# Performance work log

Measured on AMD Instinct MI355X. Metric: run time of the kernel, lower is better.

The kernel has to match this reference:

```python
import jax, jax.numpy as jnp
import numpy as np

B, T, C, H = 2, 2048, 1024, 16
HD = C // H  # head dim = 64


def setup_inputs() -> dict:
    key = jax.random.key(0)
    k1, k2, k3, k4, k5 = jax.random.split(key, 5)
    s = 0.02
    return {
        "x": jax.random.normal(k1, (B, T, C), dtype=jnp.float32),
        "W_attn": jax.random.normal(k2, (3 * C, C), dtype=jnp.float32) * s,
        "b_attn": jax.random.normal(k3, (3 * C,), dtype=jnp.float32) * s,
        "W_proj": jax.random.normal(k4, (C, C), dtype=jnp.float32) * s,
        "b_proj": jax.random.normal(k5, (C,), dtype=jnp.float32) * s,
    }


def reference(x, W_attn, b_attn, W_proj, b_proj):
    Bs, Ts, Cs = x.shape
    # QKV projection (torch Linear: x @ W.T + b)
    qkv = x @ W_attn.T + b_attn  # (B, T, 3C)
    q, k, v = jnp.split(qkv, 3, axis=2)
    # (B, H, T, HD)
    q = q.reshape(Bs, Ts, H, HD).transpose(0, 2, 1, 3)
    k = k.reshape(Bs, Ts, H, HD).transpose(0, 2, 1, 3)
    v = v.reshape(Bs, Ts, H, HD).transpose(0, 2, 1, 3)
    scale = 1.0 / np.sqrt(HD).astype(np.float32)
    att = jnp.einsum("bhqd,bhkd->bhqk", q, k) * scale
    causal = jnp.tril(jnp.ones((Ts, Ts), dtype=bool))
    att = jnp.where(causal[None, None], att, -jnp.inf)
    att = jax.nn.softmax(att, axis=-1)
    y = jnp.einsum("bhqk,bhkd->bhqd", att, v)
    y = y.transpose(0, 2, 1, 3).reshape(Bs, Ts, Cs)
    return y @ W_proj.T + b_proj
```

## Files before the change

### kernel.cpp

```cpp
#include <hip/hip_runtime.h>


#define B_   2
#define T_   2048
#define C_   1024
#define H_   16
#define HD_  64
#define BT_  (B_ * T_)
#define C3_  (3 * C_)
#define NT_  (T_ / 64)
#define SCL_ 0.18033688f

typedef __attribute__((ext_vector_type(8))) __bf16 bf16x8;
typedef __attribute__((ext_vector_type(4))) float  f32x4;
typedef __attribute__((ext_vector_type(8))) unsigned short u16x8;

__device__ __forceinline__ unsigned short f2bf(float f) {
    unsigned int u = __float_as_uint(f);
    u = (u + 0x7fffu + ((u >> 16) & 1u)) >> 16;
    return (unsigned short)u;
}
__device__ __forceinline__ unsigned short bfc(float f) {
    return __builtin_bit_cast(unsigned short, (__bf16)f);
}

__device__ __forceinline__ size_t vphys(size_t idx) {
    return (idx >> 10) * 3072 + 2048 + (idx & 1023);
}

#define NX8  (BT_ * C_ / 8)
#define NWA8 (C3_ * C_ / 8)
#define NWP8 (C_ * C_ / 8)
#define NB8  (C3_ / 8)
#define NTOT (NX8 + NWA8 + NWP8 + NB8)
__global__ __launch_bounds__(256) void cvt3(const float* __restrict__ x,
                                            const float* __restrict__ wa,
                                            const float* __restrict__ wp,
                                            const float* __restrict__ ba,
                                            unsigned short* __restrict__ ox,
                                            unsigned short* __restrict__ owa,
                                            unsigned short* __restrict__ owp,
                                            float* __restrict__ obs) {
    int i = blockIdx.x * 256 + threadIdx.x;
    if (i >= NTOT) return;
    if (i >= NX8 + NWA8 + NWP8) {
        int jb = i - (NX8 + NWA8 + NWP8);
        int e  = jb * 8;
        float s = (e < C_) ? SCL_ : 1.0f;
        const float4* p = (const float4*)(ba + e);
        float4 f0 = p[0], f1 = p[1];
        float4* o = (float4*)(obs + e);
        o[0] = make_float4(f0.x * s, f0.y * s, f0.z * s, f0.w * s);
        o[1] = make_float4(f1.x * s, f1.y * s, f1.z * s, f1.w * s);
        return;
    }
    const float* in;
    unsigned short* out;
    int j;
    float s = 1.0f;
    if (i < NX8)             { in = x;  out = ox;  j = i; }
    else if (i < NX8 + NWA8) { in = wa; out = owa; j = i - NX8;
                               if (j < NWP8) s = SCL_; }
    else                     { in = wp; out = owp; j = i - NX8 - NWA8; }
    const float4* p = (const float4*)in;
    float4 f0 = p[j * 2];
    float4 f1 = p[j * 2 + 1];
    u16x8 o;
    o[0] = f2bf(f0.x * s); o[1] = f2bf(f0.y * s); o[2] = f2bf(f0.z * s); o[3] = f2bf(f0.w * s);
    o[4] = f2bf(f1.x * s); o[5] = f2bf(f1.y * s); o[6] = f2bf(f1.z * s); o[7] = f2bf(f1.w * s);
    ((u16x8*)out)[j] = o;
}

template<int OUT_BF16, int VSPLIT>
__global__ __launch_bounds__(256) void gemm_bt(const unsigned short* __restrict__ A,
                                               const unsigned short* __restrict__ Bm,
                                               const float* __restrict__ bias,
                                               void* __restrict__ Cv,
                                               int M, int N, int K, int nbx) {
    __shared__ __align__(16) unsigned short As[128][72];
    __shared__ __align__(16) unsigned short Bs[128][72];

    const int t    = threadIdx.x;
    const int lane = t & 63;
    const int w    = t >> 6;
    const int wr   = w & 1;
    const int wc   = w >> 1;
    const int l15  = lane & 15;
    const int lhi  = lane >> 4;

    const int nwg = gridDim.x;
    const int q8  = nwg >> 3;
    const int lin = (int)(blockIdx.x & 7) * q8 + (int)(blockIdx.x >> 3);
    const int bx  = lin % nbx;
    const int by  = lin / nbx;
    const int m0  = by * 128;
    const int n0  = bx * 128;

    f32x4 acc[4][4] = {};

    const int nk = K >> 6;
    for (int kb = 0; kb < nk; ++kb) {
        __syncthreads();
        #pragma unroll
        for (int i = 0; i < 4; ++i) {
            int g   = i * 256 + t;
            int row = g >> 3;
            int kc  = g & 7;
            uint4 va = *(const uint4*)(A  + (size_t)(m0 + row) * K + kb * 64 + kc * 8);
            *(uint4*)(&As[row][kc * 8]) = va;
            uint4 vb = *(const uint4*)(Bm + (size_t)(n0 + row) * K + kb * 64 + kc * 8);
            *(uint4*)(&Bs[row][kc * 8]) = vb;
        }
        __syncthreads();
        #pragma unroll
        for (int kk = 0; kk < 2; ++kk) {
            bf16x8 af[4], bfm[4];
            #pragma unroll
            for (int m = 0; m < 4; ++m)
                af[m] = *(const bf16x8*)(&As[wr * 64 + m * 16 + l15][kk * 32 + lhi * 8]);
            #pragma unroll
            for (int n = 0; n < 4; ++n)
                bfm[n] = *(const bf16x8*)(&Bs[wc * 64 + n * 16 + l15][kk * 32 + lhi * 8]);
            #pragma unroll
            for (int m = 0; m < 4; ++m)
                #pragma unroll
                for (int n = 0; n < 4; ++n)
                    acc[m][n] = __builtin_amdgcn_mfma_f32_16x16x32_bf16(af[m], bfm[n], acc[m][n], 0, 0, 0);
        }
    }

    if (VSPLIT && n0 >= 2048) {
        #pragma unroll
        for (int n = 0; n < 4; ++n) {
            int cg = n0 + wc * 64 + n * 16 + l15;
            float bv = bias[cg];
            int d_ = cg - 2048;
            int hh = d_ >> 6;
            int dd = d_ & 63;
            #pragma unroll
            for (int m = 0; m < 4; ++m) {
                int rg0 = m0 + wr * 64 + m * 16 + lhi * 4;
                int bb  = rg0 >> 11;
                int tt  = rg0 & 2047;
                size_t idx = ((size_t)((bb * 16 + hh) * 64 + dd)) * 2048 + tt;
                unsigned short* dst = (unsigned short*)Cv + vphys(idx);
                uint2 pk;
                pk.x = (unsigned int)f2bf(acc[m][n][0] + bv) |
                       ((unsigned int)f2bf(acc[m][n][1] + bv) << 16);
                pk.y = (unsigned int)f2bf(acc[m][n][2] + bv) |
                       ((unsigned int)f2bf(acc[m][n][3] + bv) << 16);
                *(uint2*)dst = pk;
            }
        }
    } else {
        #pragma unroll
        for (int n = 0; n < 4; ++n) {
            int cg = n0 + wc * 64 + n * 16 + l15;
            float bv = bias[cg];
            #pragma unroll
            for (int m = 0; m < 4; ++m) {
                #pragma unroll
                for (int i = 0; i < 4; ++i) {
                    int rg  = m0 + wr * 64 + m * 16 + lhi * 4 + i;
                    float v = acc[m][n][i] + bv;
                    if (OUT_BF16)
                        ((unsigned short*)Cv)[(size_t)rg * N + cg] = f2bf(v);
                    else
                        ((float*)Cv)[(size_t)rg * N + cg] = v;
                }
            }
        }
    }
}

__global__ __launch_bounds__(256) void attn_fwd(const unsigned short* __restrict__ qkv,
                                                unsigned short* __restrict__ y) {
    __shared__ __align__(16) unsigned short Ks[128][72];
    __shared__ __align__(16) unsigned short Vt[64][136];

    const int t    = threadIdx.x;
    const int lane = t & 63;
    const int wv   = t >> 6;
    const int l15  = lane & 15;
    const int lhi  = lane >> 4;
    const int b    = blockIdx.y >> 4;
    const int h    = blockIdx.y & 15;
    const size_t rowbase = (size_t)b * T_ * C3_;
    const int hoff = h * HD_;
    unsigned short* PsW = &Ks[0][0] + wv * (16 * 136);

    const unsigned short* krow = qkv + rowbase + C_ + hoff;
    const size_t vIdx0 = ((size_t)(b * 16 + h) * 64) * 2048;

    #pragma unroll 1
    for (int half = 0; half < 2; ++half) {
        const int qt = half ? (NT_ - 1 - (int)blockIdx.x) : (int)blockIdx.x;
        const int q0 = qt * 64;

        bf16x8 qf[2];
        {
            int qrow = q0 + wv * 16 + l15;
            const unsigned short* qp = qkv + rowbase + (size_t)qrow * C3_ + hoff + lhi * 8;
            qf[0] = *(const bf16x8*)(qp);
            qf[1] = *(const bf16x8*)(qp + 32);
        }

        float Mx = -1e30f, Lx = 0.f;
        f32x4 oacc[4];
        #pragma unroll
        for (int n = 0; n < 4; ++n) oacc[n] = f32x4{0.f, 0.f, 0.f, 0.f};

        const int niter = (qt + 2) >> 1;
        for (int it = 0; it < niter; ++it) {
            const int k0 = it * 128;
            __syncthreads();
            #pragma unroll
            for (int i = 0; i < 4; ++i) {
                int g   = i * 256 + t;
                int row = g >> 3;
                int kc  = g & 7;
                *(uint4*)(&Ks[row][kc * 8]) =
                    *(const uint4*)(krow + (size_t)(k0 + row) * C3_ + kc * 8);
            }
            #pragma unroll
            for (int i = 0; i < 4; ++i) {
                int g  = i * 256 + t;
                int dd = g >> 4;
                int kc = g & 15;
                size_t idx = vIdx0 + (size_t)dd * 2048 + k0 + kc * 8;
                *(u16x8*)(&Vt[dd][kc * 8]) = *(const u16x8*)(qkv + vphys(idx));
            }
            __syncthreads();

            f32x4 sacc[8];
            #pragma unroll
            for (int n = 0; n < 8; ++n) sacc[n] = f32x4{0.f, 0.f, 0.f, 0.f};
            __builtin_amdgcn_s_setprio(1);
            #pragma unroll
            for (int kk = 0; kk < 2; ++kk) {
                #pragma unroll
                for (int n = 0; n < 8; ++n) {
                    bf16x8 kf = *(const bf16x8*)(&Ks[n * 16 + l15][kk * 32 + lhi * 8]);
                    sacc[n] = __builtin_amdgcn_mfma_f32_16x16x32_bf16(kf, qf[kk], sacc[n], 0, 0, 0);
                }
            }
            __builtin_amdgcn_s_setprio(0);
            __syncthreads();

            const int qg = q0 + wv * 16 + l15;
            if (k0 + 127 > q0) {
                #pragma unroll
                for (int n = 0; n < 8; ++n) {
                    int kg = k0 + n * 16 + lhi * 4;
                    #pragma unroll
                    for (int r = 0; r < 4; ++r)
                        sacc[n][r] = (kg + r <= qg) ? sacc[n][r] : -1e30f;
                }
            }

            float vmx = sacc[0][0];
            #pragma unroll
            for (int n = 0; n < 8; ++n)
                #pragma unroll
                for (int r = 0; r < 4; ++r) vmx = fmaxf(vmx, sacc[n][r]);
            vmx = fmaxf(vmx, __shfl_xor(vmx, 16));
            vmx = fmaxf(vmx, __shfl_xor(vmx, 32));
            float Mn = fmaxf(Mx, vmx);
            float al = exp2f(Mx - Mn);
            Mx = Mn;
            float rs = 0.f;
            #pragma unroll
            for (int n = 0; n < 8; ++n)
                #pragma unroll
                for (int r = 0; r < 4; ++r) {
                    float e = exp2f(sacc[n][r] - Mn);
                    sacc[n][r] = e;
                    rs += e;
                }
            rs += __shfl_xor(rs, 16);
            rs += __shfl_xor(rs, 32);
            Lx = Lx * al + rs;

            #pragma unroll
            for (int r = 0; r < 4; ++r) {
                float ar = __shfl(al, lhi * 4 + r);
                #pragma unroll
                for (int nd = 0; nd < 4; ++nd) oacc[nd][r] *= ar;
            }

            #pragma unroll
            for (int n = 0; n < 8; ++n) {
                unsigned int lo = (unsigned int)bfc(sacc[n][0]) | ((unsigned int)bfc(sacc[n][1]) << 16);
                unsigned int hi = (unsigned int)bfc(sacc[n][2]) | ((unsigned int)bfc(sacc[n][3]) << 16);
                uint2 pk; pk.x = lo; pk.y = hi;
                *(uint2*)(PsW + l15 * 136 + n * 16 + lhi * 4) = pk;
            }
            asm volatile("s_waitcnt lgkmcnt(0)" ::: "memory");

            __builtin_amdgcn_s_setprio(1);
            #pragma unroll
            for (int kk = 0; kk < 4; ++kk) {
                bf16x8 pf = *(const bf16x8*)(PsW + l15 * 136 + kk * 32 + lhi * 8);
                #pragma unroll
                for (int nd = 0; nd < 4; ++nd) {
                    bf16x8 vf = *(const bf16x8*)(&Vt[nd * 16 + l15][kk * 32 + lhi * 8]);
                    oacc[nd] = __builtin_amdgcn_mfma_f32_16x16x32_bf16(pf, vf, oacc[nd], 0, 0, 0);
                }
            }
            __builtin_amdgcn_s_setprio(0);
        }

        #pragma unroll
        for (int i = 0; i < 4; ++i) {
            float Lr = __shfl(Lx, lhi * 4 + i);
            float rL = 1.0f / Lr;
            #pragma unroll
            for (int nd = 0; nd < 4; ++nd) {
                int qg = q0 + wv * 16 + lhi * 4 + i;
                y[(size_t)(b * T_ + qg) * C_ + hoff + nd * 16 + l15] = bfc(oacc[nd][i] * rL);
            }
        }
    }
}

extern "C" void kernel_launch(void* const* d_in, const int* in_sizes, int n_in,
                              void* d_out, int out_size, void* d_ws, size_t ws_size,
                              hipStream_t stream) {
    const float* x      = (const float*)d_in[0];
    const float* W_attn = (const float*)d_in[1];
    const float* b_attn = (const float*)d_in[2];
    const float* W_proj = (const float*)d_in[3];
    const float* b_proj = (const float*)d_in[4];
    float* out = (float*)d_out;

    char* ws = (char*)d_ws;
    unsigned short* xb   = (unsigned short*)(ws);
    unsigned short* wab  = (unsigned short*)(ws + 8388608);
    unsigned short* wpb  = (unsigned short*)(ws + 8388608 + 6291456);
    unsigned short* qkvb = (unsigned short*)(ws + 16777216);
    unsigned short* yb   = (unsigned short*)(ws + 16777216 + 25165824);
    float*          bs   = (float*)(ws + 16777216 + 25165824 + 8388608);

    cvt3<<<(NTOT + 255) / 256, 256, 0, stream>>>(x, W_attn, W_proj, b_attn, xb, wab, wpb, bs);

    gemm_bt<1, 1><<<(C3_ / 128) * (BT_ / 128), 256, 0, stream>>>(xb, wab, bs, qkvb, BT_, C3_, C_, C3_ / 128);

    attn_fwd<<<dim3(NT_ / 2, B_ * H_), 256, 0, stream>>>(qkvb, yb);

    gemm_bt<0, 0><<<(C_ / 128) * (BT_ / 128), 256, 0, stream>>>(yb, wpb, b_proj, out, BT_, C_, C_, C_ / 128);
}
```

Before: 211.0 us.

## Swizzle attention LDS tiles into fragment order and remap blocks across XCDs

Replaces the padded row-major K and transposed-V shared-memory tiles with an XOR-swizzled layout. Each MFMA fragment read becomes a contiguous 16-byte load at a precomputed offset, and the P scratch uses the same scheme. The aim is to cut LDS bank conflicts and address arithmetic in the inner loop. The grid also becomes 1D with a block-index permutation, so neighbouring head/query-pair blocks are spread across the XCDs, and a sched_barrier is added before the PV MFMAs. The risk is more complex store addressing and swizzle bugs.

```diff
diff --git a/kernel.cpp b/kernel.cpp
--- a/kernel.cpp
+++ b/kernel.cpp
@@ -175,34 +175,45 @@
 
 __global__ __launch_bounds__(256) void attn_fwd(const unsigned short* __restrict__ qkv,
                                                 unsigned short* __restrict__ y) {
-    __shared__ __align__(16) unsigned short Ks[128][72];
-    __shared__ __align__(16) unsigned short Vt[64][136];
+    __shared__ __align__(16) unsigned short KL[8192];
+    __shared__ __align__(16) unsigned short VL[8192];
 
     const int t    = threadIdx.x;
     const int lane = t & 63;
     const int wv   = t >> 6;
     const int l15  = lane & 15;
     const int lhi  = lane >> 4;
-    const int b    = blockIdx.y >> 4;
-    const int h    = blockIdx.y & 15;
+
+    const int bid = blockIdx.x;
+    const int idx = (bid >> 3) + (bid & 7) * 64;
+    const int bh  = idx >> 4;
+    const int qp  = idx & 15;
+    const int b   = bh >> 4;
+    const int h   = bh & 15;
     const size_t rowbase = (size_t)b * T_ * C3_;
     const int hoff = h * HD_;
-    unsigned short* PsW = &Ks[0][0] + wv * (16 * 136);
+
+    unsigned short* Pw = KL + wv * 2048;
+
+    int voff[4];
+    #pragma unroll
+    for (int kk = 0; kk < 4; ++kk)
+        voff[kk] = ((kk * 4 + lhi) * 16 + (l15 ^ lhi ^ ((kk & 1) << 2))) * 8;
 
     const unsigned short* krow = qkv + rowbase + C_ + hoff;
     const size_t vIdx0 = ((size_t)(b * 16 + h) * 64) * 2048;
 
     #pragma unroll 1
     for (int half = 0; half < 2; ++half) {
-        const int qt = half ? (NT_ - 1 - (int)blockIdx.x) : (int)blockIdx.x;
+        const int qt = half ? (NT_ - 1 - qp) : qp;
         const int q0 = qt * 64;
 
         bf16x8 qf[2];
         {
             int qrow = q0 + wv * 16 + l15;
-            const unsigned short* qp = qkv + rowbase + (size_t)qrow * C3_ + hoff + lhi * 8;
-            qf[0] = *(const bf16x8*)(qp);
-            qf[1] = *(const bf16x8*)(qp + 32);
+            const unsigned short* qp_ = qkv + rowbase + (size_t)qrow * C3_ + hoff + lhi * 8;
+            qf[0] = *(const bf16x8*)(qp_);
+            qf[1] = *(const bf16x8*)(qp_ + 32);
         }
 
         float Mx = -1e30f, Lx = 0.f;
@@ -217,18 +228,20 @@
             #pragma unroll
             for (int i = 0; i < 4; ++i) {
                 int g   = i * 256 + t;
-                int row = g >> 3;
-                int kc  = g & 7;
-                *(uint4*)(&Ks[row][kc * 8]) =
-                    *(const uint4*)(krow + (size_t)(k0 + row) * C3_ + kc * 8);
+                int row = g >> 3, cc = g & 7;
+                int n_ = row >> 4, f15 = row & 15, fkk = cc >> 2, fhi = cc & 3;
+                int slot = ((n_ * 2 + fkk) * 4 + fhi) * 16 + (f15 ^ fhi ^ ((fkk & 1) << 2));
+                *(u16x8*)(KL + slot * 8) =
+                    *(const u16x8*)(krow + (size_t)(k0 + row) * C3_ + cc * 8);
             }
             #pragma unroll
             for (int i = 0; i < 4; ++i) {
                 int g  = i * 256 + t;
-                int dd = g >> 4;
-                int kc = g & 15;
-                size_t idx = vIdx0 + (size_t)dd * 2048 + k0 + kc * 8;
-                *(u16x8*)(&Vt[dd][kc * 8]) = *(const u16x8*)(qkv + vphys(idx));
+                int d  = g >> 4, kc = g & 15;
+                int nd = d >> 4, f15 = d & 15, fkk = kc >> 2, fhi = kc & 3;
+                int slot = ((nd * 4 + fkk) * 4 + fhi) * 16 + (f15 ^ fhi ^ ((fkk & 1) << 2));
+                size_t gidx = vIdx0 + (size_t)d * 2048 + k0 + kc * 8;
+                *(u16x8*)(VL + slot * 8) = *(const u16x8*)(qkv + vphys(gidx));
             }
             __syncthreads();
 
@@ -240,7 +253,7 @@
             for (int kk = 0; kk < 2; ++kk) {
                 #pragma unroll
                 for (int n = 0; n < 8; ++n) {
-                    bf16x8 kf = *(const bf16x8*)(&Ks[n * 16 + l15][kk * 32 + lhi * 8]);
+                    bf16x8 kf = *(const bf16x8*)(KL + n * 1024 + voff[kk]);
                     sacc[n] = __builtin_amdgcn_mfma_f32_16x16x32_bf16(kf, qf[kk], sacc[n], 0, 0, 0);
                 }
             }
@@ -290,20 +303,25 @@
 
             #pragma unroll
             for (int n = 0; n < 8; ++n) {
-                unsigned int lo = (unsigned int)bfc(sacc[n][0]) | ((unsigned int)bfc(sacc[n][1]) << 16);
-                unsigned int hi = (unsigned int)bfc(sacc[n][2]) | ((unsigned int)bfc(sacc[n][3]) << 16);
-                uint2 pk; pk.x = lo; pk.y = hi;
-                *(uint2*)(PsW + l15 * 136 + n * 16 + lhi * 4) = pk;
+                const int kkR  = n >> 1;
+                const int lhiR = ((n & 1) << 1) | (lhi >> 1);
+                const int j0   = (lhi & 1) * 4;
+                const int slot = (kkR * 4 + lhiR) * 16 + (l15 ^ lhiR ^ ((kkR & 1) << 2));
+                uint2 pk;
+                pk.x = (unsigned int)bfc(sacc[n][0]) | ((unsigned int)bfc(sacc[n][1]) << 16);
+                pk.y = (unsigned int)bfc(sacc[n][2]) | ((unsigned int)bfc(sacc[n][3]) << 16);
+                *(uint2*)(Pw + slot * 8 + j0) = pk;
             }
             asm volatile("s_waitcnt lgkmcnt(0)" ::: "memory");
+            __builtin_amdgcn_sched_barrier(0);
 
             __builtin_amdgcn_s_setprio(1);
             #pragma unroll
             for (int kk = 0; kk < 4; ++kk) {
-                bf16x8 pf = *(const bf16x8*)(PsW + l15 * 136 + kk * 32 + lhi * 8);
+                bf16x8 pf = *(const bf16x8*)(Pw + voff[kk]);
                 #pragma unroll
                 for (int nd = 0; nd < 4; ++nd) {
-                    bf16x8 vf = *(const bf16x8*)(&Vt[nd * 16 + l15][kk * 32 + lhi * 8]);
+                    bf16x8 vf = *(const bf16x8*)(VL + nd * 2048 + voff[kk]);
                     oacc[nd] = __builtin_amdgcn_mfma_f32_16x16x32_bf16(pf, vf, oacc[nd], 0, 0, 0);
                 }
             }
@@ -345,7 +363,7 @@
 
     gemm_bt<1, 1><<<(C3_ / 128) * (BT_ / 128), 256, 0, stream>>>(xb, wab, bs, qkvb, BT_, C3_, C_, C3_ / 128);
 
-    attn_fwd<<<dim3(NT_ / 2, B_ * H_), 256, 0, stream>>>(qkvb, yb);
+    attn_fwd<<<512, 256, 0, stream>>>(qkvb, yb);
 
     gemm_bt<0, 0><<<(C_ / 128) * (BT_ / 128), 256, 0, stream>>>(yb, wpb, b_proj, out, BT_, C_, C_, C_ / 128);
 }
```

Result: faster. 204.6 us (-3.1%).
